# Kernel optimization log

Hardware: AMD Instinct MI355X
Metric: run time of the kernel (lower is better)

## Reference

```python
import jax, jax.numpy as jnp
import numpy as np

H = 8          # number of heads
D_MODEL = 512  # model dim
D_HEAD = D_MODEL // H


def setup_inputs() -> dict:
    key = jax.random.key(0)
    ks = jax.random.split(key, 8)
    B, C, L = 4, D_MODEL, 2048
    s = 1.0 / np.sqrt(D_MODEL)
    return {
        "x1": jax.random.normal(ks[0], (B, C, L), dtype=jnp.float32),
        "x2": jax.random.normal(ks[1], (B, C, L), dtype=jnp.float32),
        "Wq": jax.random.uniform(ks[2], (D_MODEL, D_MODEL), jnp.float32, -s, s),
        "bq": jax.random.uniform(ks[3], (D_MODEL,), jnp.float32, -s, s),
        "Wk": jax.random.uniform(ks[4], (D_MODEL, D_MODEL), jnp.float32, -s, s),
        "bk": jax.random.uniform(ks[5], (D_MODEL,), jnp.float32, -s, s),
        "Wv": jax.random.uniform(ks[6], (D_MODEL, D_MODEL), jnp.float32, -s, s),
        "bv": jax.random.uniform(ks[7], (D_MODEL,), jnp.float32, -s, s),
    }


def reference(x1, x2, Wq, bq, Wk, bk, Wv, bv):
    # x1, x2: [B, C, L] with C == d_model (3D branch of the torch module)
    B, C, L = x1.shape
    x1t = jnp.swapaxes(x1, 1, 2)  # [B, L, C]
    x2t = jnp.swapaxes(x2, 1, 2)  # [B, L, C]

    def proj(x, W, b):  # torch Linear: x @ W.T + b, then split heads
        y = jnp.einsum('blc,dc->bld', x, W) + b          # [B, L, C]
        return y.reshape(B, -1, H, D_HEAD).transpose(0, 2, 1, 3)  # [B, H, L, d]

    q = proj(x1t, Wq, bq)
    k = proj(x2t, Wk, bk)
    v = proj(x2t, Wv, bv)

    scores = jnp.einsum('bhqd,bhkd->bhqk', q, k) / jnp.sqrt(
        jnp.asarray(D_HEAD, dtype=q.dtype))
    attn = jax.nn.softmax(scores, axis=-1)
    out = jnp.einsum('bhqk,bhkd->bhqd', attn, v)          # [B, H, L, d]

    # transpose(1,2).view(B,-1,C).transpose(1,2) -> [B, C, L]
    out = out.transpose(0, 2, 1, 3).reshape(B, L, C)
    return jnp.swapaxes(out, 1, 2)
```

## Files before the change

### kernel.cpp

```cpp
#include <hip/hip_runtime.h>
#include <hip/hip_bf16.h>

#define L_SEQ 2048
#define DM 512

typedef short bf16x8 __attribute__((ext_vector_type(8)));
typedef float f32x4 __attribute__((ext_vector_type(4)));
typedef float f32x16 __attribute__((ext_vector_type(16)));
typedef unsigned short u16;
typedef u16 u16x8 __attribute__((ext_vector_type(8)));
typedef u16 u16x4 __attribute__((ext_vector_type(4)));
typedef unsigned int u32x2 __attribute__((ext_vector_type(2)));

__device__ __forceinline__ u16 f2bf(float f) {
    unsigned int u = __float_as_uint(f);
    u += 0x7fffu + ((u >> 16) & 1u);
    return (u16)(u >> 16);
}

__device__ __forceinline__ unsigned int pk_bf16(float a, float b) {
    __hip_bfloat162 h = __float22bfloat162_rn(float2{a, b});
    unsigned int u;
    __builtin_memcpy(&u, &h, 4);
    return u;
}

__device__ __forceinline__ void lds_load16(const void* g, void* l) {
    __builtin_amdgcn_global_load_lds(
        (const __attribute__((address_space(1))) unsigned int*)g,
        (__attribute__((address_space(3))) unsigned int*)l,
        16, 0, 0);
}

__device__ __forceinline__ f32x16 zero16() {
    f32x16 z;
#pragma unroll
    for (int i = 0; i < 16; ++i) z[i] = 0.f;
    return z;
}

__global__ void prep(const float* __restrict__ x1, const float* __restrict__ x2,
                     const float* __restrict__ Wq, const float* __restrict__ Wk,
                     const float* __restrict__ Wv,
                     u16* __restrict__ xT, u16* __restrict__ Wall) {
    __shared__ u16 t[128 * 136];
    const int tid = threadIdx.x;
    if (blockIdx.z == 8) {
        int gid = (blockIdx.y * 16 + blockIdx.x) * 256 + tid;
#pragma unroll
        for (int p = 0; p < 12; ++p) {
            int i = p * 16384 + gid;
            int which = i >> 16, j = i & 65535;
            const float* src = (which == 0) ? Wq : (which == 1 ? Wk : Wv);
            float4 v = ((const float4*)src)[j];
            ushort4 o;
            o.x = f2bf(v.x); o.y = f2bf(v.y); o.z = f2bf(v.z); o.w = f2bf(v.w);
            ((ushort4*)Wall)[i] = o;
        }
        return;
    }
    const int z = blockIdx.z, b = z & 3, c0 = blockIdx.y * 128, l0 = blockIdx.x * 128;
    const float* src = (z < 4) ? x1 : x2;
    u16* dbase = xT + (size_t)(z >> 2) * 4194304;
    const float* sp = src + ((size_t)b * DM + c0) * L_SEQ + l0;
#pragma unroll
    for (int p = 0; p < 16; ++p) {
        int id = p * 256 + tid;
        int ci = id >> 5, f4 = id & 31;
        float4 v = *(const float4*)(sp + (size_t)ci * L_SEQ + f4 * 4);
        u16x4 o;
        o[0] = f2bf(v.x); o[1] = f2bf(v.y); o[2] = f2bf(v.z); o[3] = f2bf(v.w);
        *(u16x4*)(t + ci * 136 + f4 * 4) = o;
    }
    __syncthreads();
    u16* dp = dbase + ((size_t)b * L_SEQ + l0) * DM + c0;
#pragma unroll
    for (int p = 0; p < 8; ++p) {
        int id = p * 256 + tid;
        int lj = id >> 4, c8 = id & 15;
        u16x8 o;
#pragma unroll
        for (int i = 0; i < 8; ++i) o[i] = t[(c8 * 8 + i) * 136 + lj];
        *(u16x8*)(dp + (size_t)lj * DM + c8 * 8) = o;
    }
}

#define PROJ_BODY(AB, BB, NAB, NBB, DO_STAGE)                                   \
    {                                                                           \
        __syncthreads();                                                        \
        if (DO_STAGE) {                                                         \
            lds_load16(pA0, smem + (NAB) + sd0);                                \
            lds_load16(pA1, smem + (NAB) + sd1);                                \
            lds_load16(pB0, smem + (NBB) + sd0);                                \
            lds_load16(pB1, smem + (NBB) + sd1);                                \
            pA0 += 32; pA1 += 32; pB0 += 32; pB1 += 32;                         \
        }                                                                       \
        bf16x8 af[4], bfr[4];                                                   \
        _Pragma("unroll")                                                       \
        for (int mt = 0; mt < 4; ++mt)                                          \
            af[mt] = *(const bf16x8*)(smem + (AB) + aoffb[mt]);                 \
        _Pragma("unroll")                                                       \
        for (int nt = 0; nt < 4; ++nt)                                          \
            bfr[nt] = *(const bf16x8*)(smem + (BB) + boffb[nt]);                \
        _Pragma("unroll")                                                       \
        for (int mt = 0; mt < 4; ++mt)                                          \
            _Pragma("unroll")                                                   \
            for (int nt = 0; nt < 4; ++nt)                                      \
                acc[mt][nt] = __builtin_amdgcn_mfma_f32_16x16x32_bf16(          \
                    af[mt], bfr[nt], acc[mt][nt], 0, 0, 0);                     \
    }

__launch_bounds__(256, 3)
__global__ void proj_gemm(const u16* __restrict__ x1T, const u16* __restrict__ x2T,
                          const u16* __restrict__ Wall,
                          const float* __restrict__ bq, const float* __restrict__ bk,
                          const float* __restrict__ bv,
                          u16* __restrict__ Qo, u16* __restrict__ Ko, u16* __restrict__ Vto) {
    __shared__ __align__(16) char smem[34816];
    const int by = blockIdx.y;
    const int b = by / 3, pj = by % 3;
    const int m0 = (blockIdx.x >> 2) * 128, n0 = (blockIdx.x & 3) * 128;
    const u16* xT = (pj == 0) ? x1T : x2T;
    const u16* W = Wall + (size_t)pj * 262144;
    const float* bias = (pj == 0) ? bq : (pj == 1 ? bk : bv);
    const float scale = (pj == 0) ? 0.18033688011112042f : 1.0f;

    const int tid = threadIdx.x;
    const int w = tid >> 6, lane = tid & 63;
    const int lm = lane & 15, lq = lane >> 4;
    const int wrow = (w & 1) * 64, wcol = (w >> 1) * 64;

    const u16 *pA0, *pA1, *pB0, *pB1;
    {
        int s0 = tid, r0 = s0 >> 2, c0 = (s0 & 3) ^ (r0 & 3);
        int s1 = 256 + tid, r1 = s1 >> 2, c1 = (s1 & 3) ^ (r1 & 3);
        pA0 = xT + ((size_t)b * L_SEQ + m0 + r0) * DM + c0 * 8;
        pA1 = xT + ((size_t)b * L_SEQ + m0 + r1) * DM + c1 * 8;
        pB0 = W + (size_t)(n0 + r0) * DM + c0 * 8;
        pB1 = W + (size_t)(n0 + r1) * DM + c1 * 8;
    }
    const int sd0 = w * 1024;
    const int sd1 = 4096 + w * 1024;

    int aoffb[4], boffb[4];
#pragma unroll
    for (int mt = 0; mt < 4; ++mt) {
        int r = wrow + mt * 16 + lm;
        aoffb[mt] = r * 64 + (lq ^ (r & 3)) * 16;
    }
#pragma unroll
    for (int nt = 0; nt < 4; ++nt) {
        int r = wcol + nt * 16 + lm;
        boffb[nt] = r * 64 + (lq ^ (r & 3)) * 16;
    }

    f32x4 acc[4][4];
#pragma unroll
    for (int mt = 0; mt < 4; ++mt)
#pragma unroll
        for (int nt = 0; nt < 4; ++nt) acc[mt][nt] = (f32x4){0.f, 0.f, 0.f, 0.f};

    lds_load16(pA0, smem + 0 + sd0);
    lds_load16(pA1, smem + 0 + sd1);
    lds_load16(pB0, smem + 8192 + sd0);
    lds_load16(pB1, smem + 8192 + sd1);
    pA0 += 32; pA1 += 32; pB0 += 32; pB1 += 32;

    for (int kt2 = 0; kt2 < 8; ++kt2) {
        PROJ_BODY(0, 8192, 16384, 24576, true)
        PROJ_BODY(16384, 24576, 0, 8192, (kt2 < 7))
    }

    float bvv[4];
#pragma unroll
    for (int nt = 0; nt < 4; ++nt) bvv[nt] = bias[n0 + wcol + nt * 16 + lm];

    if (pj < 2) {
        u16* dst = (pj == 0) ? Qo : Ko;
#pragma unroll
        for (int mt = 0; mt < 4; ++mt)
#pragma unroll
            for (int nt = 0; nt < 4; ++nt) {
                int col = n0 + wcol + nt * 16 + lm;
#pragma unroll
                for (int r = 0; r < 4; ++r) {
                    int row = m0 + wrow + mt * 16 + lq * 4 + r;
                    dst[((size_t)b * L_SEQ + row) * DM + col] = f2bf((acc[mt][nt][r] + bvv[nt]) * scale);
                }
            }
    } else {
        __syncthreads();
        u16* epi = (u16*)smem;
#pragma unroll
        for (int mt = 0; mt < 4; ++mt)
#pragma unroll
            for (int nt = 0; nt < 4; ++nt) {
                int colL = wcol + nt * 16 + lm;
                int row0 = wrow + mt * 16 + lq * 4;
                u16x4 tv;
#pragma unroll
                for (int r = 0; r < 4; ++r) tv[r] = f2bf(acc[mt][nt][r] + bvv[nt]);
                *(u16x4*)(epi + colL * 136 + row0) = tv;
            }
        __syncthreads();
#pragma unroll
        for (int p = 0; p < 8; ++p) {
            int id = p * 256 + tid;
            int rr = id >> 4, ch = id & 15;
            u16x8 vv = *(const u16x8*)(epi + rr * 136 + ch * 8);
            *(u16x8*)(Vto + ((size_t)b * DM + n0 + rr) * L_SEQ + m0 + ch * 8) = vv;
        }
    }
}

#define ATTN_BODY(KB, VB, NKB, NVB, DO_STAGE)                                   \
    {                                                                           \
        __syncthreads();                                                        \
        if (DO_STAGE) {                                                         \
            lds_load16(pKn, smem + (NKB) + sdb);                                \
            lds_load16(pVn, smem + (NVB) + sdb);                                \
            pKn += 64 * DM; pVn += 64;                                          \
        }                                                                       \
        bf16x8 af0 = *(const bf16x8*)(smem + (KB) + koffb[0]);                  \
        f32x16 s = __builtin_amdgcn_mfma_f32_32x32x16_bf16(af0, qf[0], z16,     \
                                                           0, 0, 0);            \
        _Pragma("unroll")                                                       \
        for (int c = 1; c < 4; ++c) {                                           \
            bf16x8 af = *(const bf16x8*)(smem + (KB) + koffb[c]);               \
            s = __builtin_amdgcn_mfma_f32_32x32x16_bf16(af, qf[c], s, 0, 0, 0); \
        }                                                                       \
        uint2 pw[4];                                                            \
        _Pragma("unroll")                                                       \
        for (int g2 = 0; g2 < 4; ++g2) {                                        \
            float p0 = __builtin_amdgcn_exp2f(s[4 * g2 + 0]);                   \
            float p1 = __builtin_amdgcn_exp2f(s[4 * g2 + 1]);                   \
            float p2 = __builtin_amdgcn_exp2f(s[4 * g2 + 2]);                   \
            float p3 = __builtin_amdgcn_exp2f(s[4 * g2 + 3]);                   \
            l_part += (p0 + p1) + (p2 + p3);                                    \
            pw[g2].x = pk_bf16(p0, p1);                                         \
            pw[g2].y = pk_bf16(p2, p3);                                         \
        }                                                                       \
        _Pragma("unroll")                                                       \
        for (int c2 = 0; c2 < 2; ++c2) {                                        \
            uint2 pa = pw[2 * c2], pb = pw[2 * c2 + 1];                         \
            u32x2 rx = __builtin_amdgcn_permlane32_swap(pa.x, pb.x, false, false); \
            u32x2 ry = __builtin_amdgcn_permlane32_swap(pa.y, pb.y, false, false); \
            uint4 pu;                                                           \
            pu.x = rx[0]; pu.y = ry[0]; pu.z = rx[1]; pu.w = ry[1];             \
            bf16x8 pf;                                                          \
            __builtin_memcpy(&pf, &pu, 16);                                     \
            _Pragma("unroll")                                                   \
            for (int dt = 0; dt < 2; ++dt) {                                    \
                bf16x8 vf = *(const bf16x8*)(smem + (VB) + voffb[c2 * 2 + dt]); \
                o_acc[dt] = __builtin_amdgcn_mfma_f32_32x32x16_bf16(            \
                    pf, vf, o_acc[dt], 0, 0, 0);                                \
            }                                                                   \
        }                                                                       \
    }

__launch_bounds__(512, 4)
__global__ void attn(const u16* __restrict__ Q, const u16* __restrict__ K,
                     const u16* __restrict__ Vt, float* __restrict__ out) {
    __shared__ __align__(16) char smem[34816];
    float* l_lds = (float*)(smem + 33792);
    float* o_lds = (float*)smem;

    const int i = blockIdx.x;
    const int g = i & 7, r_ = i >> 3;
    const int qb = r_ & 15, bh = ((r_ >> 4) << 3) + g;
    const int h_ = bh >> 2, b = bh & 3;

    const int tid = threadIdx.x, w = tid >> 6, lane = tid & 63;
    const int q0 = qb * 128;
    const int lm32 = lane & 31, hi = lane >> 5;
    const int qg = w & 3, hk = w >> 2;
    const int qrow = qg * 32 + lm32;

    const u16* Qb = Q + ((size_t)b * L_SEQ + q0) * DM + h_ * 64;
    const u16* Kb = K + (size_t)b * L_SEQ * DM + h_ * 64;
    const u16* Vb = Vt + ((size_t)b * DM + h_ * 64) * L_SEQ;

    const u16 *pKn, *pVn;
    const int sdb = w * 1024;
    {
        int r = tid >> 3, cc = (tid & 7) ^ (r & 7);
        pKn = Kb + (size_t)r * DM + cc * 8;
        pVn = Vb + (size_t)r * L_SEQ + cc * 8;
    }

    const int rk = hk * 32 + lm32;
    int koffb[4], voffb[4];
#pragma unroll
    for (int c = 0; c < 4; ++c)
        koffb[c] = rk * 128 + ((2 * c + hi) ^ (rk & 7)) * 16;
#pragma unroll
    for (int c2 = 0; c2 < 2; ++c2)
#pragma unroll
        for (int dt = 0; dt < 2; ++dt) {
            int d = dt * 32 + lm32;
            int kc = hk * 4 + c2 * 2 + hi;
            voffb[c2 * 2 + dt] = d * 128 + (kc ^ (d & 7)) * 16;
        }

#pragma unroll
    for (int j = 0; j < 2; ++j) {
        int s = j * 512 + tid;
        int r = s >> 3, cc = (s & 7) ^ (r & 7);
        lds_load16(Qb + (size_t)r * DM + cc * 8, smem + j * 8192 + sdb);
    }
    __syncthreads();
    bf16x8 qf[4];
#pragma unroll
    for (int c = 0; c < 4; ++c) {
        int slot = (2 * c + hi) ^ (qrow & 7);
        qf[c] = *(const bf16x8*)(smem + qrow * 128 + slot * 16);
    }
    __syncthreads();

    float l_part = 0.f;
    const f32x16 z16 = zero16();
    f32x16 o_acc[2];
    o_acc[0] = zero16(); o_acc[1] = zero16();

    lds_load16(pKn, smem + 0 + sdb);
    lds_load16(pVn, smem + 16384 + sdb);
    pKn += 64 * DM; pVn += 64;

    for (int kt2 = 0; kt2 < 16; ++kt2) {
        ATTN_BODY(0, 16384, 8192, 24576, true)
        ATTN_BODY(8192, 24576, 0, 16384, (kt2 < 15))
    }

    l_part += __shfl_xor(l_part, 32);

    __syncthreads();
    if (hi == 0) l_lds[hk * 128 + qrow] = l_part;
    if (hk == 0) {
#pragma unroll
        for (int dt = 0; dt < 2; ++dt) {
            int d = dt * 32 + lm32;
#pragma unroll
            for (int g2 = 0; g2 < 4; ++g2) {
                f32x4 vq;
#pragma unroll
                for (int r = 0; r < 4; ++r) vq[r] = o_acc[dt][4 * g2 + r];
                *(f32x4*)(o_lds + d * 132 + qg * 32 + 8 * g2 + 4 * hi) = vq;
            }
        }
    }
    __syncthreads();
    if (hk == 1) {
#pragma unroll
        for (int dt = 0; dt < 2; ++dt) {
            int d = dt * 32 + lm32;
#pragma unroll
            for (int g2 = 0; g2 < 4; ++g2) {
                float* ad = o_lds + d * 132 + qg * 32 + 8 * g2 + 4 * hi;
                f32x4 cur = *(f32x4*)ad;
#pragma unroll
                for (int r = 0; r < 4; ++r) cur[r] += o_acc[dt][4 * g2 + r];
                *(f32x4*)ad = cur;
            }
        }
    }
    __syncthreads();
    float* ob = out + ((size_t)b * DM + h_ * 64) * L_SEQ + q0;
#pragma unroll
    for (int p = 0; p < 4; ++p) {
        int id = p * 512 + tid;
        int d = id >> 5, rc = id & 31;
        f32x4 vv = *(const f32x4*)(o_lds + d * 132 + rc * 4);
        f32x4 la = *(const f32x4*)(l_lds + rc * 4);
        f32x4 lb = *(const f32x4*)(l_lds + 128 + rc * 4);
#pragma unroll
        for (int j = 0; j < 4; ++j) vv[j] *= 1.0f / (la[j] + lb[j]);
        *(f32x4*)(ob + (size_t)d * L_SEQ + rc * 4) = vv;
    }
}

extern "C" void kernel_launch(void* const* d_in, const int* in_sizes, int n_in,
                              void* d_out, int out_size, void* d_ws, size_t ws_size,
                              hipStream_t stream) {
    const float* x1 = (const float*)d_in[0];
    const float* x2 = (const float*)d_in[1];
    const float* Wq = (const float*)d_in[2];
    const float* bq = (const float*)d_in[3];
    const float* Wk = (const float*)d_in[4];
    const float* bk = (const float*)d_in[5];
    const float* Wv = (const float*)d_in[6];
    const float* bv = (const float*)d_in[7];
    float* out = (float*)d_out;

    char* ws = (char*)d_ws;
    u16* x1T = (u16*)(ws);
    u16* x2T = (u16*)(ws + 8388608);
    u16* Wall = (u16*)(ws + 16777216);
    u16* Qb  = (u16*)(ws + 18350080);
    u16* Kb  = (u16*)(ws + 26738688);
    u16* Vtb = (u16*)(ws + 35127296);

    prep<<<dim3(16, 4, 9), 256, 0, stream>>>(x1, x2, Wq, Wk, Wv, x1T, Wall);
    proj_gemm<<<dim3(64, 12), 256, 0, stream>>>(x1T, x2T, Wall, bq, bk, bv, Qb, Kb, Vtb);
    attn<<<512, 512, 0, stream>>>(Qb, Kb, Vtb, out);
}
```

Before: 164.3 us.

## Triple-buffer K/V LDS staging with explicit vmcnt waits and MFMA priority

Moves the attention K/V staging from double to triple buffering, with three tiles prefetched before the loop. A tile's refill is now issued after its compute, and explicit s_waitcnt vmcnt waits plus raw barriers replace the implicit syncthreads. It also raises wave priority around the MFMA sections with s_setprio. The goal is to hide global-to-LDS latency better; the cost is more LDS per block (about 49KB), which may limit occupancy at 4 blocks per CU.

```diff
diff --git a/kernel.cpp b/kernel.cpp
--- a/kernel.cpp
+++ b/kernel.cpp
@@ -213,15 +213,12 @@
     }
 }
 
-#define ATTN_BODY(KB, VB, NKB, NVB, DO_STAGE)                                   \
+#define ATTN_BODY(KB, VB, VMC, DO_STAGE)                                        \
     {                                                                           \
-        __syncthreads();                                                        \
-        if (DO_STAGE) {                                                         \
-            lds_load16(pKn, smem + (NKB) + sdb);                                \
-            lds_load16(pVn, smem + (NVB) + sdb);                                \
-            pKn += 64 * DM; pVn += 64;                                          \
-        }                                                                       \
+        asm volatile("s_waitcnt vmcnt(" #VMC ")" ::: "memory");                 \
+        __builtin_amdgcn_s_barrier();                                           \
         bf16x8 af0 = *(const bf16x8*)(smem + (KB) + koffb[0]);                  \
+        __builtin_amdgcn_s_setprio(1);                                          \
         f32x16 s = __builtin_amdgcn_mfma_f32_32x32x16_bf16(af0, qf[0], z16,     \
                                                            0, 0, 0);            \
         _Pragma("unroll")                                                       \
@@ -229,6 +226,7 @@
             bf16x8 af = *(const bf16x8*)(smem + (KB) + koffb[c]);               \
             s = __builtin_amdgcn_mfma_f32_32x32x16_bf16(af, qf[c], s, 0, 0, 0); \
         }                                                                       \
+        __builtin_amdgcn_s_setprio(0);                                          \
         uint2 pw[4];                                                            \
         _Pragma("unroll")                                                       \
         for (int g2 = 0; g2 < 4; ++g2) {                                        \
@@ -240,6 +238,7 @@
             pw[g2].x = pk_bf16(p0, p1);                                         \
             pw[g2].y = pk_bf16(p2, p3);                                         \
         }                                                                       \
+        __builtin_amdgcn_s_setprio(1);                                          \
         _Pragma("unroll")                                                       \
         for (int c2 = 0; c2 < 2; ++c2) {                                        \
             uint2 pa = pw[2 * c2], pb = pw[2 * c2 + 1];                         \
@@ -256,13 +255,21 @@
                     pf, vf, o_acc[dt], 0, 0, 0);                                \
             }                                                                   \
         }                                                                       \
+        __builtin_amdgcn_s_setprio(0);                                          \
+        asm volatile("s_waitcnt lgkmcnt(0)" ::: "memory");                      \
+        __builtin_amdgcn_s_barrier();                                           \
+        if (DO_STAGE) {                                                         \
+            lds_load16(pKn, smem + (KB) + sdb);                                 \
+            lds_load16(pVn, smem + (VB) + sdb);                                 \
+            pKn += 64 * DM; pVn += 64;                                          \
+        }                                                                       \
     }
 
 __launch_bounds__(512, 4)
 __global__ void attn(const u16* __restrict__ Q, const u16* __restrict__ K,
                      const u16* __restrict__ Vt, float* __restrict__ out) {
-    __shared__ __align__(16) char smem[34816];
-    float* l_lds = (float*)(smem + 33792);
+    __shared__ __align__(16) char smem[50176];
+    float* l_lds = (float*)(smem + 49152);
     float* o_lds = (float*)smem;
 
     const int i = blockIdx.x;
@@ -322,14 +329,17 @@
     f32x16 o_acc[2];
     o_acc[0] = zero16(); o_acc[1] = zero16();
 
-    lds_load16(pKn, smem + 0 + sdb);
-    lds_load16(pVn, smem + 16384 + sdb);
-    pKn += 64 * DM; pVn += 64;
-
-    for (int kt2 = 0; kt2 < 16; ++kt2) {
-        ATTN_BODY(0, 16384, 8192, 24576, true)
-        ATTN_BODY(8192, 24576, 0, 16384, (kt2 < 15))
-    }
+    lds_load16(pKn, smem + 0 + sdb);     lds_load16(pVn, smem + 24576 + sdb); pKn += 64 * DM; pVn += 64;
+    lds_load16(pKn, smem + 8192 + sdb);  lds_load16(pVn, smem + 32768 + sdb); pKn += 64 * DM; pVn += 64;
+    lds_load16(pKn, smem + 16384 + sdb); lds_load16(pVn, smem + 40960 + sdb); pKn += 64 * DM; pVn += 64;
+
+    for (int kt3 = 0; kt3 < 10; ++kt3) {
+        ATTN_BODY(0,     24576, 4, true)
+        ATTN_BODY(8192,  32768, 4, true)
+        ATTN_BODY(16384, 40960, 4, (kt3 < 9))
+    }
+    ATTN_BODY(0,    24576, 2, false)
+    ATTN_BODY(8192, 32768, 0, false)
 
     l_part += __shfl_xor(l_part, 32);
 
```

Result: faster. 160.6 us (-2.3%).

## Halve attention query tile to 64 rows with 256-thread blocks and MFMA priority hints

Applied to the files above, without the earlier changes.

The attention kernel now runs 1024 blocks of 256 threads, each covering 64 query rows instead of 128. Each thread issues two async K/V tile loads per stage because there are fewer threads. The output staging and row-sum buffers shrink to match. s_setprio hints raise wave priority around the MFMA sections to help interleave waves. More blocks give finer-grained occupancy, but K/V traffic per query row doubles since each K/V tile is reused by fewer queries.

```diff
diff --git a/kernel.cpp b/kernel.cpp
--- a/kernel.cpp
+++ b/kernel.cpp
@@ -217,11 +217,14 @@
     {                                                                           \
         __syncthreads();                                                        \
         if (DO_STAGE) {                                                         \
-            lds_load16(pKn, smem + (NKB) + sdb);                                \
-            lds_load16(pVn, smem + (NVB) + sdb);                                \
-            pKn += 64 * DM; pVn += 64;                                          \
+            lds_load16(pK0, smem + (NKB) + sdb);                                \
+            lds_load16(pK1, smem + (NKB) + 4096 + sdb);                         \
+            lds_load16(pV0, smem + (NVB) + sdb);                                \
+            lds_load16(pV1, smem + (NVB) + 4096 + sdb);                         \
+            pK0 += 64 * DM; pK1 += 64 * DM; pV0 += 64; pV1 += 64;               \
         }                                                                       \
         bf16x8 af0 = *(const bf16x8*)(smem + (KB) + koffb[0]);                  \
+        __builtin_amdgcn_s_setprio(1);                                          \
         f32x16 s = __builtin_amdgcn_mfma_f32_32x32x16_bf16(af0, qf[0], z16,     \
                                                            0, 0, 0);            \
         _Pragma("unroll")                                                       \
@@ -229,6 +232,7 @@
             bf16x8 af = *(const bf16x8*)(smem + (KB) + koffb[c]);               \
             s = __builtin_amdgcn_mfma_f32_32x32x16_bf16(af, qf[c], s, 0, 0, 0); \
         }                                                                       \
+        __builtin_amdgcn_s_setprio(0);                                          \
         uint2 pw[4];                                                            \
         _Pragma("unroll")                                                       \
         for (int g2 = 0; g2 < 4; ++g2) {                                        \
@@ -240,11 +244,11 @@
             pw[g2].x = pk_bf16(p0, p1);                                         \
             pw[g2].y = pk_bf16(p2, p3);                                         \
         }                                                                       \
+        __builtin_amdgcn_s_setprio(1);                                          \
         _Pragma("unroll")                                                       \
         for (int c2 = 0; c2 < 2; ++c2) {                                        \
-            uint2 pa = pw[2 * c2], pb = pw[2 * c2 + 1];                         \
-            u32x2 rx = __builtin_amdgcn_permlane32_swap(pa.x, pb.x, false, false); \
-            u32x2 ry = __builtin_amdgcn_permlane32_swap(pa.y, pb.y, false, false); \
+            u32x2 rx = __builtin_amdgcn_permlane32_swap(pw[2 * c2].x, pw[2 * c2 + 1].x, false, false); \
+            u32x2 ry = __builtin_amdgcn_permlane32_swap(pw[2 * c2].y, pw[2 * c2 + 1].y, false, false); \
             uint4 pu;                                                           \
             pu.x = rx[0]; pu.y = ry[0]; pu.z = rx[1]; pu.w = ry[1];             \
             bf16x8 pf;                                                          \
@@ -256,36 +260,39 @@
                     pf, vf, o_acc[dt], 0, 0, 0);                                \
             }                                                                   \
         }                                                                       \
-    }
-
-__launch_bounds__(512, 4)
+        __builtin_amdgcn_s_setprio(0);                                          \
+    }
+
+__launch_bounds__(256, 4)
 __global__ void attn(const u16* __restrict__ Q, const u16* __restrict__ K,
                      const u16* __restrict__ Vt, float* __restrict__ out) {
-    __shared__ __align__(16) char smem[34816];
-    float* l_lds = (float*)(smem + 33792);
+    __shared__ __align__(16) char smem[33280];
+    float* l_lds = (float*)(smem + 32768);
     float* o_lds = (float*)smem;
 
     const int i = blockIdx.x;
     const int g = i & 7, r_ = i >> 3;
-    const int qb = r_ & 15, bh = ((r_ >> 4) << 3) + g;
+    const int qb = r_ & 31, bh = ((r_ >> 5) << 3) + g;
     const int h_ = bh >> 2, b = bh & 3;
 
     const int tid = threadIdx.x, w = tid >> 6, lane = tid & 63;
-    const int q0 = qb * 128;
+    const int q0 = qb * 64;
     const int lm32 = lane & 31, hi = lane >> 5;
-    const int qg = w & 3, hk = w >> 2;
+    const int qg = w & 1, hk = w >> 1;
     const int qrow = qg * 32 + lm32;
 
     const u16* Qb = Q + ((size_t)b * L_SEQ + q0) * DM + h_ * 64;
     const u16* Kb = K + (size_t)b * L_SEQ * DM + h_ * 64;
     const u16* Vb = Vt + ((size_t)b * DM + h_ * 64) * L_SEQ;
 
-    const u16 *pKn, *pVn;
+    const u16 *pK0, *pK1, *pV0, *pV1;
     const int sdb = w * 1024;
     {
         int r = tid >> 3, cc = (tid & 7) ^ (r & 7);
-        pKn = Kb + (size_t)r * DM + cc * 8;
-        pVn = Vb + (size_t)r * L_SEQ + cc * 8;
+        pK0 = Kb + (size_t)r * DM + cc * 8;
+        pK1 = Kb + (size_t)(32 + r) * DM + cc * 8;
+        pV0 = Vb + (size_t)r * L_SEQ + cc * 8;
+        pV1 = Vb + (size_t)(32 + r) * L_SEQ + cc * 8;
     }
 
     const int rk = hk * 32 + lm32;
@@ -304,9 +311,9 @@
 
 #pragma unroll
     for (int j = 0; j < 2; ++j) {
-        int s = j * 512 + tid;
+        int s = j * 256 + tid;
         int r = s >> 3, cc = (s & 7) ^ (r & 7);
-        lds_load16(Qb + (size_t)r * DM + cc * 8, smem + j * 8192 + sdb);
+        lds_load16(Qb + (size_t)r * DM + cc * 8, smem + j * 4096 + sdb);
     }
     __syncthreads();
     bf16x8 qf[4];
@@ -322,9 +329,11 @@
     f32x16 o_acc[2];
     o_acc[0] = zero16(); o_acc[1] = zero16();
 
-    lds_load16(pKn, smem + 0 + sdb);
-    lds_load16(pVn, smem + 16384 + sdb);
-    pKn += 64 * DM; pVn += 64;
+    lds_load16(pK0, smem + 0 + sdb);
+    lds_load16(pK1, smem + 4096 + sdb);
+    lds_load16(pV0, smem + 16384 + sdb);
+    lds_load16(pV1, smem + 16384 + 4096 + sdb);
+    pK0 += 64 * DM; pK1 += 64 * DM; pV0 += 64; pV1 += 64;
 
     for (int kt2 = 0; kt2 < 16; ++kt2) {
         ATTN_BODY(0, 16384, 8192, 24576, true)
@@ -334,7 +343,7 @@
     l_part += __shfl_xor(l_part, 32);
 
     __syncthreads();
-    if (hi == 0) l_lds[hk * 128 + qrow] = l_part;
+    if (hi == 0) l_lds[hk * 64 + qrow] = l_part;
     if (hk == 0) {
 #pragma unroll
         for (int dt = 0; dt < 2; ++dt) {
@@ -344,7 +353,7 @@
                 f32x4 vq;
 #pragma unroll
                 for (int r = 0; r < 4; ++r) vq[r] = o_acc[dt][4 * g2 + r];
-                *(f32x4*)(o_lds + d * 132 + qg * 32 + 8 * g2 + 4 * hi) = vq;
+                *(f32x4*)(o_lds + d * 68 + qg * 32 + 8 * g2 + 4 * hi) = vq;
             }
         }
     }
@@ -355,7 +364,7 @@
             int d = dt * 32 + lm32;
 #pragma unroll
             for (int g2 = 0; g2 < 4; ++g2) {
-                float* ad = o_lds + d * 132 + qg * 32 + 8 * g2 + 4 * hi;
+                float* ad = o_lds + d * 68 + qg * 32 + 8 * g2 + 4 * hi;
                 f32x4 cur = *(f32x4*)ad;
 #pragma unroll
                 for (int r = 0; r < 4; ++r) cur[r] += o_acc[dt][4 * g2 + r];
@@ -367,11 +376,11 @@
     float* ob = out + ((size_t)b * DM + h_ * 64) * L_SEQ + q0;
 #pragma unroll
     for (int p = 0; p < 4; ++p) {
-        int id = p * 512 + tid;
-        int d = id >> 5, rc = id & 31;
-        f32x4 vv = *(const f32x4*)(o_lds + d * 132 + rc * 4);
+        int id = p * 256 + tid;
+        int d = id >> 4, rc = id & 15;
+        f32x4 vv = *(const f32x4*)(o_lds + d * 68 + rc * 4);
         f32x4 la = *(const f32x4*)(l_lds + rc * 4);
-        f32x4 lb = *(const f32x4*)(l_lds + 128 + rc * 4);
+        f32x4 lb = *(const f32x4*)(l_lds + 64 + rc * 4);
 #pragma unroll
         for (int j = 0; j < 4; ++j) vv[j] *= 1.0f / (la[j] + lb[j]);
         *(f32x4*)(ob + (size_t)d * L_SEQ + rc * 4) = vv;
@@ -401,5 +410,5 @@
 
     prep<<<dim3(16, 4, 9), 256, 0, stream>>>(x1, x2, Wq, Wk, Wv, x1T, Wall);
     proj_gemm<<<dim3(64, 12), 256, 0, stream>>>(x1T, x2T, Wall, bq, bk, bv, Qb, Kb, Vtb);
-    attn<<<512, 512, 0, stream>>>(Qb, Kb, Vtb, out);
-}
+    attn<<<1024, 256, 0, stream>>>(Qb, Kb, Vtb, out);
+}
```

After: 167.0 us. Within noise of the previous version (+1.6%).
